# Performance work log

Hardware: AMD Instinct MI355X
Metric: run time of the kernel (lower is better)

## Reference

```python
import jax, jax.numpy as jnp
import numpy as np

DIM = 1024
HEADS = 16
DIM_HEAD = 64
INNER = HEADS * DIM_HEAD  # 1024
B, N = 4, 1024
SCALE = DIM_HEAD ** -0.5


def _layernorm(t, g, b, eps=1e-5):
    mu = jnp.mean(t, axis=-1, keepdims=True)
    var = jnp.var(t, axis=-1, keepdims=True)
    return (t - mu) * jax.lax.rsqrt(var + eps) * g + b


def setup_inputs() -> dict:
    key = jax.random.key(0)
    ks = jax.random.split(key, 8)
    return {
        "x": jax.random.normal(ks[0], (B, N, DIM), dtype=jnp.float32),
        "y": jax.random.normal(ks[1], (B, N, DIM), dtype=jnp.float32),
        "gx": jnp.ones((DIM,), jnp.float32),
        "bx": jnp.zeros((DIM,), jnp.float32),
        "gy": jnp.ones((DIM,), jnp.float32),
        "by": jnp.zeros((DIM,), jnp.float32),
        "Wqkv_x": jax.random.normal(ks[2], (DIM, 3 * INNER), jnp.float32) * 0.02,
        "Wqkv_y": jax.random.normal(ks[3], (DIM, 3 * INNER), jnp.float32) * 0.02,
        "Wout_x": jax.random.normal(ks[4], (INNER, DIM), jnp.float32) * 0.02,
        "bout_x": jnp.zeros((DIM,), jnp.float32),
        "Wout_y": jax.random.normal(ks[5], (INNER, DIM), jnp.float32) * 0.02,
        "bout_y": jnp.zeros((DIM,), jnp.float32),
    }


def _split_heads(t):
    b, n, _ = t.shape
    return t.reshape(b, n, HEADS, DIM_HEAD).transpose(0, 2, 1, 3)  # b h n d


def reference(x, y, gx, bx, gy, by, Wqkv_x, Wqkv_y, Wout_x, bout_x, Wout_y, bout_y):
    xn = _layernorm(x, gx, bx)
    yn = _layernorm(y, gy, by)
    qx, kx, vx = [_split_heads(t) for t in jnp.split(xn @ Wqkv_x, 3, axis=-1)]
    qy, ky, vy = [_split_heads(t) for t in jnp.split(yn @ Wqkv_y, 3, axis=-1)]
    # concat along HEADS dim -> 2h heads; each stream's heads attend within that stream
    q = jnp.concatenate([qx, qy], axis=1)
    k = jnp.concatenate([kx, ky], axis=1)
    v = jnp.concatenate([vx, vy], axis=1)
    dots = jnp.einsum('bhid,bhjd->bhij', q, k) * SCALE  # [B, 2h, N, N]
    attn = jax.nn.softmax(dots, axis=-1)
    out = jnp.einsum('bhij,bhjd->bhid', attn, v)  # [B, 2h, N, d]
    xo = out[:, :HEADS]  # original code uses the x-chunk for BOTH outputs (faithful)
    xo = xo.transpose(0, 2, 1, 3).reshape(xo.shape[0], xo.shape[2], INNER)  # b n (h d)
    out_x = xo @ Wout_x + bout_x
    out_y = xo @ Wout_y + bout_y
    return (out_x, out_y)
```

## Files before the change

### kernel.cpp

```cpp
#include <hip/hip_runtime.h>

typedef __attribute__((ext_vector_type(8))) short s16x8;
typedef __attribute__((ext_vector_type(4))) float f32x4;
typedef unsigned short u16;

#define DEV __device__ __forceinline__

DEV u16 f2bf(float f) {
    unsigned u = __builtin_bit_cast(unsigned, f);
    unsigned r = u + 0x7fffu + ((u >> 16) & 1u);
    return (u16)(r >> 16);
}

DEV float exp2a(float x) {
    float r;
    asm("v_exp_f32 %0, %1" : "=v"(r) : "v"(x));
    return r;
}

DEV unsigned cvtpk(float lo, float hi) {
    unsigned r;
    asm("v_cvt_pk_bf16_f32 %0, %1, %2" : "=v"(r) : "v"(lo), "v"(hi));
    return r;
}

DEV void gload_lds16(const void* g, void* l) {
    __builtin_amdgcn_global_load_lds(
        (const __attribute__((address_space(1))) unsigned int*)g,
        (__attribute__((address_space(3))) unsigned int*)l, 16, 0, 0);
}

DEV f32x4 mfma16(s16x8 a, s16x8 b, f32x4 c) {
    return __builtin_amdgcn_mfma_f32_16x16x32_bf16(a, b, c, 0, 0, 0);
}

template <int N>
DEV void vmwait() {
    asm volatile("s_waitcnt vmcnt(%0)" ::"n"(N) : "memory");
}

__global__ __launch_bounds__(256) void ln_kernel(const float* __restrict__ x,
                                                 const float* __restrict__ g,
                                                 const float* __restrict__ b,
                                                 u16* __restrict__ xn) {
    const int row = blockIdx.x, t = threadIdx.x;
    const float4 v = *(const float4*)(x + (size_t)row * 1024 + t * 4);
    float s1 = v.x + v.y + v.z + v.w;
    float s2 = v.x * v.x + v.y * v.y + v.z * v.z + v.w * v.w;
#pragma unroll
    for (int d = 1; d < 64; d <<= 1) {
        s1 += __shfl_xor(s1, d);
        s2 += __shfl_xor(s2, d);
    }
    __shared__ float red[8];
    if ((t & 63) == 0) { red[(t >> 6) * 2] = s1; red[(t >> 6) * 2 + 1] = s2; }
    __syncthreads();
    s1 = red[0] + red[2] + red[4] + red[6];
    s2 = red[1] + red[3] + red[5] + red[7];
    const float mu = s1 * (1.0f / 1024.0f);
    const float var = s2 * (1.0f / 1024.0f) - mu * mu;
    const float rs = rsqrtf(var + 1e-5f);
    const float4 gv = *(const float4*)(g + t * 4);
    const float4 bv = *(const float4*)(b + t * 4);
    ushort4 o;
    o.x = f2bf((v.x - mu) * rs * gv.x + bv.x);
    o.y = f2bf((v.y - mu) * rs * gv.y + bv.y);
    o.z = f2bf((v.z - mu) * rs * gv.z + bv.z);
    o.w = f2bf((v.w - mu) * rs * gv.w + bv.w);
    *(ushort4*)(xn + (size_t)row * 1024 + t * 4) = o;
}

__global__ __launch_bounds__(256) void transpose_w(const float* __restrict__ src0,
                                                   const float* __restrict__ src1,
                                                   u16* __restrict__ dst, int ld) {
    __shared__ float tile[64][68];
    const int t = threadIdx.x;
    const float* src = (blockIdx.z == 0) ? src0 : src1;
    u16* d0 = dst + (size_t)blockIdx.z * 1024 * 1024;
    const int n0 = blockIdx.x * 64, k0 = blockIdx.y * 64;
    const int kl = t >> 4, nl = (t & 15) * 4;
#pragma unroll
    for (int p = 0; p < 4; ++p) {
        float4 v = *(const float4*)(src + (size_t)(k0 + kl + p * 16) * ld + n0 + nl);
        tile[kl + p * 16][nl + 0] = v.x;
        tile[kl + p * 16][nl + 1] = v.y;
        tile[kl + p * 16][nl + 2] = v.z;
        tile[kl + p * 16][nl + 3] = v.w;
    }
    __syncthreads();
    const int nl2 = t >> 2, kc = (t & 3) * 16;
    __align__(16) u16 tmp[16];
#pragma unroll
    for (int j = 0; j < 16; ++j) tmp[j] = f2bf(tile[kc + j][nl2]);
    u16* d = d0 + (size_t)(n0 + nl2) * 1024 + k0 + kc;
    ((uint4*)d)[0] = ((const uint4*)tmp)[0];
    ((uint4*)d)[1] = ((const uint4*)tmp)[1];
}

__global__ __launch_bounds__(256) void transpose_v(const u16* __restrict__ V,
                                                   u16* __restrict__ Vt) {
    __shared__ u16 tile[64][72];
    const int t = threadIdx.x;
    const int j0 = blockIdx.x * 64;
    const int bh = blockIdx.y;
    const u16* src = V + (size_t)bh * 65536;
    const int jl = t >> 4, dl = (t & 15) * 4;
#pragma unroll
    for (int p = 0; p < 4; ++p) {
        ushort4 v = *(const ushort4*)(src + (size_t)(j0 + jl + p * 16) * 64 + dl);
        *(ushort4*)&tile[jl + p * 16][dl] = v;
    }
    __syncthreads();
    const int dl2 = t >> 2, jc = (t & 3) * 16;
    __align__(16) u16 tmp[16];
#pragma unroll
    for (int j = 0; j < 16; ++j) tmp[j] = tile[jc + j][dl2];
    u16* d = Vt + (size_t)bh * 65536 + (size_t)dl2 * 1024 + j0 + jc;
    ((uint4*)d)[0] = ((const uint4*)tmp)[0];
    ((uint4*)d)[1] = ((const uint4*)tmp)[1];
}

__global__ __launch_bounds__(512, 2) void gemm1k(const u16* __restrict__ A,
                                                 const u16* __restrict__ B,
                                                 u16* __restrict__ Qb, u16* __restrict__ Kb,
                                                 u16* __restrict__ Vb) {
    constexpr int MQ = 2, NQ = 3, HA = 32, HB = 48, TM = 64, TN = 96;
    constexpr int CHA = 1024, CHBF = 1536;
    constexpr int NI = 8;

    __shared__ __align__(16) u16 As[2 * 2 * CHA * 8];
    __shared__ __align__(16) u16 Bs[2 * CHBF * 8];

    const int tid = threadIdx.x, lane = tid & 63;
    const int wave = tid >> 6;
    const int wm = wave >> 1, wn = wave & 1;
    const int lr = lane & 15, cg = lane >> 4;

    const int bid = blockIdx.x;
    const int bid2 = (bid & 7) * 32 + (bid >> 3);
    const int bxi = bid2 & 15, byi = bid2 >> 4;
    const int m0 = byi * 256, n0 = bxi * 192;

    const u16* __restrict__ Ag = A + (size_t)m0 * 1024;
    const u16* __restrict__ Bg = B + (size_t)n0 * 1024;

    f32x4 acc[2 * MQ][2 * NQ] = {};

#define STG_A(b, h, t)                                                              \
    do {                                                                            \
        _Pragma("unroll") for (int u = 0; u < 2; ++u) {                             \
            const int idx = u * 512 + tid;                                          \
            const int loc = idx >> 3, pp = idx & 7;                                 \
            const int row = (loc & 127) | ((h)*128);                                \
            gload_lds16(Ag + (size_t)row * 1024 + (t)*64 + ((pp ^ (row & 7)) << 3), \
                        &As[(((b)*2 + (h)) * CHA + idx) * 8]);                      \
        }                                                                           \
    } while (0)
#define STG_B(b, t)                                                                 \
    do {                                                                            \
        _Pragma("unroll") for (int u = 0; u < 3; ++u) {                             \
            const int idx = u * 512 + tid;                                          \
            const int row = idx >> 3, pp = idx & 7;                                 \
            gload_lds16(Bg + (size_t)row * 1024 + (t)*64 + ((pp ^ (row & 7)) << 3), \
                        &Bs[((b)*CHBF + idx) * 8]);                                 \
        }                                                                           \
    } while (0)

#define LDA(bb, lm, dst)                                                            \
    _Pragma("unroll") for (int mf = 0; mf < MQ; ++mf)                               \
        _Pragma("unroll") for (int ks = 0; ks < 2; ++ks) {                          \
            const int grow = wm * 64 + (lm)*32 + mf * 16 + lr;                      \
            dst[mf][ks] = *(const s16x8*)&As[((((bb)*2 + (grow >> 7)) * CHA) +      \
                                              (grow & 127) * 8 +                    \
                                              ((cg + ks * 4) ^ (lr & 7))) * 8];     \
        }

#define LDB(bb, ln, dst)                                                            \
    _Pragma("unroll") for (int nf = 0; nf < NQ; ++nf)                               \
        _Pragma("unroll") for (int ks = 0; ks < 2; ++ks) {                          \
            const int rr = wn * TN + (ln)*HB + nf * 16 + lr;                        \
            dst[nf][ks] = *(const s16x8*)&Bs[((bb)*CHBF + rr * 8 +                  \
                                              ((cg + ks * 4) ^ (lr & 7))) * 8];     \
        }

#define MM(lm, ln, A_, B_)                                                          \
    __builtin_amdgcn_s_setprio(1);                                                  \
    _Pragma("unroll") for (int mf = 0; mf < MQ; ++mf)                               \
        _Pragma("unroll") for (int nf = 0; nf < NQ; ++nf)                           \
            _Pragma("unroll") for (int ks = 0; ks < 2; ++ks)                        \
                acc[(lm)*MQ + mf][(ln)*NQ + nf] = mfma16(                           \
                    A_[mf][ks], B_[nf][ks], acc[(lm)*MQ + mf][(ln)*NQ + nf]);       \
    __builtin_amdgcn_s_setprio(0);

#define BAR() asm volatile("s_barrier" ::: "memory")

    STG_A(0, 0, 0);
    STG_A(0, 1, 0);
    STG_B(0, 0);
    STG_A(1, 0, 1);
    STG_B(1, 1);
    vmwait<5>();
    BAR();

    s16x8 va[MQ][2];
    s16x8 vb0[NQ][2], vb1[NQ][2];

#pragma unroll 1
    for (int i = 0; i < NI - 1; ++i) {
        const int t1 = 2 * i + 1, t2 = 2 * i + 2, t3 = 2 * i + 3;
        LDA(0, 0, va); LDB(0, 0, vb0); STG_A(1, 1, t1); BAR(); MM(0, 0, va, vb0);
        LDB(0, 1, vb1);                                 BAR(); MM(0, 1, va, vb1);
        LDA(0, 1, va);                 STG_A(0, 0, t2); BAR(); MM(1, 0, va, vb0);
        STG_B(0, t2); vmwait<5>();                      BAR(); MM(1, 1, va, vb1);
        LDA(1, 0, va); LDB(1, 0, vb0); STG_A(0, 1, t2); BAR(); MM(0, 0, va, vb0);
        LDB(1, 1, vb1);                                 BAR(); MM(0, 1, va, vb1);
        LDA(1, 1, va);                 STG_A(1, 0, t3); BAR(); MM(1, 0, va, vb0);
        STG_B(1, t3); vmwait<5>();                      BAR(); MM(1, 1, va, vb1);
    }
    LDA(0, 0, va); LDB(0, 0, vb0); STG_A(1, 1, 15); BAR(); MM(0, 0, va, vb0);
    LDB(0, 1, vb1);                                 BAR(); MM(0, 1, va, vb1);
    LDA(0, 1, va);                                  BAR(); MM(1, 0, va, vb0);
    vmwait<0>();                                    BAR(); MM(1, 1, va, vb1);
    LDA(1, 0, va); LDB(1, 0, vb0); MM(0, 0, va, vb0);
    LDB(1, 1, vb1);                MM(0, 1, va, vb1);
    LDA(1, 1, va);                 MM(1, 0, va, vb0);
    MM(1, 1, va, vb1);

#undef STG_A
#undef STG_B
#undef LDA
#undef LDB
#undef MM
#undef BAR

#pragma unroll
    for (int am = 0; am < 2 * MQ; ++am) {
        const int lm = am / MQ, mf = am % MQ;
        const int rowb = m0 + wm * TM + lm * HA + mf * 16 + cg * 4;
#pragma unroll
        for (int an = 0; an < 2 * NQ; ++an) {
            const int ln = an / NQ, nf = an % NQ;
            const int col = n0 + wn * TN + ln * HB + nf * 16 + lr;
            const int which = col >> 10, hd = col & 1023;
            const int h = hd >> 6, dd = hd & 63;
            u16* dst = (which == 0) ? Qb : (which == 1) ? Kb : Vb;
            const float sc = (which == 0) ? 0.18033688011112042f : 1.0f;
#pragma unroll
            for (int r = 0; r < 4; ++r) {
                const int tk = rowb + r;
                const int bb2 = tk >> 10, ii = tk & 1023;
                dst[(size_t)(((bb2 << 4) + h) * 1024 + ii) * 64 + dd] =
                    f2bf(acc[am][an][r] * sc);
            }
        }
    }
}

template <int BN, int WM, int EPI>
__global__ __launch_bounds__(512, 2) void gemm8(const u16* __restrict__ A,
                                                const u16* __restrict__ B,
                                                u16* __restrict__ Qb, u16* __restrict__ Kb,
                                                u16* __restrict__ Vb,
                                                const float* __restrict__ bx,
                                                const float* __restrict__ by,
                                                float* __restrict__ out, int NBX) {
    constexpr int BM = 256, WN = 8 / WM;
    constexpr int TM = BM / WM, TN = BN / WN;
    constexpr int MQ = TM / 32, NQ = TN / 32;
    constexpr int HA = TM / 2, HB = TN / 2;
    constexpr int CHA = 1024;
    constexpr int CHB = BN * 4;
    constexpr int GA = 2, GB = CHB / 512;
    constexpr int NI = 8;

    __shared__ __align__(16) u16 As[2 * 2 * CHA * 8];
    __shared__ __align__(16) u16 Bs[2 * 2 * CHB * 8];

    const int tid = threadIdx.x, lane = tid & 63;
    const int wave = tid >> 6;
    const int wm = wave / WN, wn = wave % WN;
    const int lr = lane & 15, cg = lane >> 4;

    const int nwg = NBX * 16;
    const int bid = blockIdx.x;
    const int bid2 = (bid & 7) * (nwg >> 3) + (bid >> 3);
    const int bxi = bid2 % NBX, byi = bid2 / NBX;
    const int m0 = byi * 256, n0 = bxi * BN;

    const u16* __restrict__ Ag = A + (size_t)m0 * 1024;
    const u16* __restrict__ Bg = B + (size_t)n0 * 1024;

    f32x4 acc[2 * MQ][2 * NQ] = {};

#define STG_A(b, h, t)                                                              \
    do {                                                                            \
        _Pragma("unroll") for (int u = 0; u < GA; ++u) {                            \
            const int idx = u * 512 + tid;                                          \
            const int loc = idx >> 3, pp = idx & 7;                                 \
            const int row = (loc & (HA - 1)) | ((h)*HA) | ((loc / HA) * 2 * HA);    \
            gload_lds16(Ag + (size_t)row * 1024 + (t)*64 + ((pp ^ (row & 7)) << 3), \
                        &As[(((b)*2 + (h)) * CHA + idx) * 8]);                      \
        }                                                                           \
    } while (0)
#define STG_B(b, h, t)                                                              \
    do {                                                                            \
        _Pragma("unroll") for (int u = 0; u < GB; ++u) {                            \
            const int idx = u * 512 + tid;                                          \
            const int loc = idx >> 3, pp = idx & 7;                                 \
            const int row = (loc & (HB - 1)) | ((h)*HB) | ((loc / HB) * 2 * HB);    \
            gload_lds16(Bg + (size_t)row * 1024 + (t)*64 + ((pp ^ (row & 7)) << 3), \
                        &Bs[(((b)*2 + (h)) * CHB + idx) * 8]);                      \
        }                                                                           \
    } while (0)

#define LDA(bb, lm, dst)                                                            \
    _Pragma("unroll") for (int mf = 0; mf < MQ; ++mf)                               \
        _Pragma("unroll") for (int ks = 0; ks < 2; ++ks)                            \
            dst[mf][ks] = *(const s16x8*)&As[((((bb)*2 + (lm)) * CHA) +             \
                                              (mf * 16 + lr + wm * HA) * 8 +        \
                                              ((cg + ks * 4) ^ (lr & 7))) * 8];

#define LDB(bb, ln, dst)                                                            \
    _Pragma("unroll") for (int nf = 0; nf < NQ; ++nf)                               \
        _Pragma("unroll") for (int ks = 0; ks < 2; ++ks)                            \
            dst[nf][ks] = *(const s16x8*)&Bs[((((bb)*2 + (ln)) * CHB) +             \
                                              (nf * 16 + lr + wn * HB) * 8 +        \
                                              ((cg + ks * 4) ^ (lr & 7))) * 8];

#define MM(lm, ln, A_, B_)                                                          \
    __builtin_amdgcn_s_setprio(1);                                                  \
    _Pragma("unroll") for (int mf = 0; mf < MQ; ++mf)                               \
        _Pragma("unroll") for (int nf = 0; nf < NQ; ++nf)                           \
            _Pragma("unroll") for (int ks = 0; ks < 2; ++ks)                        \
                acc[(lm)*MQ + mf][(ln)*NQ + nf] = mfma16(                           \
                    A_[mf][ks], B_[nf][ks], acc[(lm)*MQ + mf][(ln)*NQ + nf]);       \
    __builtin_amdgcn_s_setprio(0);

#define BAR() asm volatile("s_barrier" ::: "memory")

    STG_A(0, 0, 0);
    STG_A(0, 1, 0);
    STG_B(0, 0, 0);
    STG_B(0, 1, 0);
    STG_A(1, 0, 1);
    STG_B(1, 0, 1);
    vmwait<GA + GB>();
    BAR();

    s16x8 va[MQ][2];
    s16x8 vb0[NQ][2], vb1[NQ][2];

#pragma unroll 1
    for (int i = 0; i < NI - 1; ++i) {
        const int t1 = 2 * i + 1, t2 = 2 * i + 2, t3 = 2 * i + 3;
        LDA(0, 0, va); LDB(0, 0, vb0); STG_A(1, 1, t1); BAR(); MM(0, 0, va, vb0);
        LDB(0, 1, vb1);                STG_B(1, 1, t1); BAR(); MM(0, 1, va, vb1);
        LDA(0, 1, va);                 STG_A(0, 0, t2); BAR(); MM(1, 0, va, vb0);
        STG_B(0, 0, t2); vmwait<GA + GB>();             BAR(); MM(1, 1, va, vb1);
        LDA(1, 0, va); LDB(1, 0, vb0); STG_A(0, 1, t2); BAR(); MM(0, 0, va, vb0);
        LDB(1, 1, vb1);                STG_B(0, 1, t2); BAR(); MM(0, 1, va, vb1);
        LDA(1, 1, va);                 STG_A(1, 0, t3); BAR(); MM(1, 0, va, vb0);
        STG_B(1, 0, t3); vmwait<GA + GB>();             BAR(); MM(1, 1, va, vb1);
    }
    LDA(0, 0, va); LDB(0, 0, vb0); STG_A(1, 1, 15); BAR(); MM(0, 0, va, vb0);
    LDB(0, 1, vb1);                STG_B(1, 1, 15); BAR(); MM(0, 1, va, vb1);
    LDA(0, 1, va);                                  BAR(); MM(1, 0, va, vb0);
    vmwait<0>();                                    BAR(); MM(1, 1, va, vb1);
    LDA(1, 0, va); LDB(1, 0, vb0); MM(0, 0, va, vb0);
    LDB(1, 1, vb1);                MM(0, 1, va, vb1);
    LDA(1, 1, va);                 MM(1, 0, va, vb0);
    MM(1, 1, va, vb1);

#undef STG_A
#undef STG_B
#undef LDA
#undef LDB
#undef MM
#undef BAR

#pragma unroll
    for (int am = 0; am < 2 * MQ; ++am) {
        const int lm = am / MQ, mf = am % MQ;
        const int rowb = m0 + wm * TM + lm * HA + mf * 16 + cg * 4;
#pragma unroll
        for (int an = 0; an < 2 * NQ; ++an) {
            const int ln = an / NQ, nf = an % NQ;
            const int col = n0 + wn * TN + ln * HB + nf * 16 + lr;
            if (EPI == 0) {
                const int which = col >> 10, hd = col & 1023;
                const int h = hd >> 6, dd = hd & 63;
                u16* dst = (which == 0) ? Qb : (which == 1) ? Kb : Vb;
                const float sc = (which == 0) ? 0.18033688011112042f : 1.0f;
#pragma unroll
                for (int r = 0; r < 4; ++r) {
                    const int tk = rowb + r;
                    const int bb2 = tk >> 10, ii = tk & 1023;
                    dst[(size_t)(((bb2 << 4) + h) * 1024 + ii) * 64 + dd] =
                        f2bf(acc[am][an][r] * sc);
                }
            } else {
                float bias;
                float* ob;
                if (col < 1024) { bias = bx[col]; ob = out + col; }
                else { bias = by[col - 1024]; ob = out + 4194304 + (col - 1024); }
#pragma unroll
                for (int r = 0; r < 4; ++r)
                    ob[(size_t)(rowb + r) * 1024] = acc[am][an][r] + bias;
            }
        }
    }
}

__global__ __launch_bounds__(256) void attn_kernel(const u16* __restrict__ Q,
                                                   const u16* __restrict__ Kg,
                                                   const u16* __restrict__ Vt,
                                                   u16* __restrict__ xo) {
    __shared__ __align__(16) u16 Ks[3][64 * 64];
    __shared__ __align__(16) u16 Vs[3][64 * 64];
    __shared__ __align__(16) u16 Ps[4][32 * 64];
    const int tid = threadIdx.x, lane = tid & 63, w = tid >> 6;
    const int bid = blockIdx.x;
    const int bh = (bid & 7) * 8 + ((bid >> 3) & 7);
    const int qblk = bid >> 6;
    const u16* Qh = Q + (size_t)bh * 65536;
    const u16* Kh = Kg + (size_t)bh * 65536;
    const u16* Vh = Vt + (size_t)bh * 65536;
    const int lr = lane & 15, cg = lane >> 4;
    const int q0 = qblk * 128 + w * 32;
    u16* Pw = &Ps[w][0];

    s16x8 qf[2][2];
#pragma unroll
    for (int qg = 0; qg < 2; ++qg)
#pragma unroll
        for (int ks = 0; ks < 2; ++ks)
            qf[qg][ks] =
                *(const s16x8*)(Qh + (size_t)(q0 + qg * 16 + lr) * 64 + ks * 32 + cg * 8);

    f32x4 o[2][4] = {};
    float l_s[2] = {0.f, 0.f};
    float m_s[2] = {-3e38f, -3e38f};
    int ba[4];
#pragma unroll
    for (int r = 0; r < 4; ++r) ba[r] = (cg * 4 + r) * 4;

#define STAGEKV(bufi, kv0)                                                               \
    do {                                                                                 \
        _Pragma("unroll") for (int i = 0; i < 2; ++i) {                                  \
            int idx = i * 256 + tid;                                                     \
            int row = idx >> 3, p = idx & 7;                                             \
            gload_lds16(Kh + (size_t)((kv0) + row) * 64 + ((p ^ (row & 7)) << 3),        \
                        &Ks[bufi][idx * 8]);                                             \
            gload_lds16(Vh + (size_t)row * 1024 + (kv0) + ((p ^ (row & 7)) << 3),        \
                        &Vs[bufi][idx * 8]);                                             \
        }                                                                                \
    } while (0)

    STAGEKV(0, 0);
    STAGEKV(1, 64);

    int buf = 0, sbuf = 2;
    for (int t = 0; t < 16; ++t) {
        if (t == 15) { vmwait<0>(); } else { vmwait<4>(); }
        asm volatile("s_barrier" ::: "memory");
        if (t < 14) STAGEKV(sbuf, (t + 2) * 64);

        f32x4 s[2][4] = {};
#pragma unroll
        for (int fn = 0; fn < 4; ++fn) {
            const int r = fn * 16 + lr;
#pragma unroll
            for (int ks = 0; ks < 2; ++ks) {
                const int c = cg + ks * 4;
                s16x8 kf = *(const s16x8*)&Ks[buf][r * 64 + ((c ^ (r & 7)) << 3)];
                s[0][fn] = mfma16(kf, qf[0][ks], s[0][fn]);
                s[1][fn] = mfma16(kf, qf[1][ks], s[1][fn]);
            }
        }

#pragma unroll
        for (int qg = 0; qg < 2; ++qg) {
            float tm = -3e38f;
#pragma unroll
            for (int fn = 0; fn < 4; ++fn)
#pragma unroll
                for (int r = 0; r < 4; ++r) tm = fmaxf(tm, s[qg][fn][r]);
            tm = fmaxf(tm, __shfl_xor(tm, 16));
            tm = fmaxf(tm, __shfl_xor(tm, 32));
            if (!__all(tm <= m_s[qg] + 8.0f)) {
                const float mn = fmaxf(m_s[qg], tm);
                const float corr = exp2a(m_s[qg] - mn);
                m_s[qg] = mn;
                l_s[qg] *= corr;
                f32x4 corr_o;
#pragma unroll
                for (int r = 0; r < 4; ++r)
                    corr_o[r] = __builtin_bit_cast(
                        float,
                        __builtin_amdgcn_ds_bpermute(ba[r], __builtin_bit_cast(int, corr)));
#pragma unroll
                for (int fd = 0; fd < 4; ++fd) o[qg][fd] *= corr_o;
            }
            const float mn = m_s[qg];
            float rs = 0.f;
            const int prow = (qg * 16 + lr) * 64;
#pragma unroll
            for (int fn = 0; fn < 4; ++fn) {
                const float p0 = exp2a(s[qg][fn][0] - mn);
                const float p1 = exp2a(s[qg][fn][1] - mn);
                const float p2 = exp2a(s[qg][fn][2] - mn);
                const float p3 = exp2a(s[qg][fn][3] - mn);
                rs += (p0 + p1) + (p2 + p3);
                uint2 dd;
                dd.x = cvtpk(p0, p1);
                dd.y = cvtpk(p2, p3);
                *(uint2*)(Pw + prow + (((2 * fn + (cg >> 1)) ^ (lr & 7)) << 3) +
                          ((cg & 1) << 2)) = dd;
            }
            rs += __shfl_xor(rs, 16);
            rs += __shfl_xor(rs, 32);
            l_s[qg] += rs;
        }

        s16x8 pf[2][2];
#pragma unroll
        for (int qg = 0; qg < 2; ++qg)
#pragma unroll
            for (int ks = 0; ks < 2; ++ks)
                pf[qg][ks] = *(const s16x8*)(Pw + (qg * 16 + lr) * 64 +
                                             (((4 * ks + cg) ^ (lr & 7)) << 3));
#pragma unroll
        for (int fd = 0; fd < 4; ++fd) {
            const int rr = fd * 16 + lr;
#pragma unroll
            for (int ks = 0; ks < 2; ++ks) {
                const int c = cg + ks * 4;
                s16x8 vf = *(const s16x8*)&Vs[buf][rr * 64 + ((c ^ (rr & 7)) << 3)];
                o[0][fd] = mfma16(pf[0][ks], vf, o[0][fd]);
                o[1][fd] = mfma16(pf[1][ks], vf, o[1][fd]);
            }
        }
        buf = (buf == 2) ? 0 : buf + 1;
        sbuf = (sbuf == 2) ? 0 : sbuf + 1;
    }
#undef STAGEKV

    const int b = bh >> 4, h = bh & 15;
#pragma unroll
    for (int qg = 0; qg < 2; ++qg) {
        f32x4 inv;
#pragma unroll
        for (int r = 0; r < 4; ++r) {
            const float lq = __builtin_bit_cast(
                float, __builtin_amdgcn_ds_bpermute(ba[r], __builtin_bit_cast(int, l_s[qg])));
            inv[r] = 1.0f / lq;
        }
#pragma unroll
        for (int r = 0; r < 4; ++r) {
            const int qrow = q0 + qg * 16 + cg * 4 + r;
#pragma unroll
            for (int fd = 0; fd < 4; ++fd)
                xo[(size_t)(b * 1024 + qrow) * 1024 + h * 64 + fd * 16 + lr] =
                    f2bf(o[qg][fd][r] * inv[r]);
        }
    }
}

extern "C" void kernel_launch(void* const* d_in, const int* in_sizes, int n_in,
                              void* d_out, int out_size, void* d_ws, size_t ws_size,
                              hipStream_t stream) {
    const float* x = (const float*)d_in[0];
    const float* gx = (const float*)d_in[2];
    const float* bxv = (const float*)d_in[3];
    const float* Wqkv = (const float*)d_in[6];
    const float* Woutx = (const float*)d_in[8];
    const float* boutx = (const float*)d_in[9];
    const float* Wouty = (const float*)d_in[10];
    const float* bouty = (const float*)d_in[11];
    float* out = (float*)d_out;

    u16* ws = (u16*)d_ws;
    u16* xn = ws;
    u16* wqkv_t = xn + 4096 * 1024;
    u16* wout_t = wqkv_t + 3072 * 1024;
    u16* Qb = wout_t + 2048 * 1024;
    u16* Kb = Qb + 64 * 1024 * 64;
    u16* Vb = Kb + 64 * 1024 * 64;
    u16* Vtb = Vb + 64 * 1024 * 64;
    u16* xob = Vtb + 64 * 1024 * 64;

    ln_kernel<<<4096, 256, 0, stream>>>(x, gx, bxv, xn);
    transpose_w<<<dim3(48, 16, 1), 256, 0, stream>>>(Wqkv, nullptr, wqkv_t, 3072);
    transpose_w<<<dim3(16, 16, 2), 256, 0, stream>>>(Woutx, Wouty, wout_t, 1024);
    gemm1k<<<256, 512, 0, stream>>>(xn, wqkv_t, Qb, Kb, Vb);
    transpose_v<<<dim3(16, 64), 256, 0, stream>>>(Vb, Vtb);
    attn_kernel<<<512, 256, 0, stream>>>(Qb, Kb, Vtb, xob);
    gemm8<128, 4, 1><<<256, 512, 0, stream>>>(xob, wout_t, nullptr, nullptr, nullptr,
                                              boutx, bouty, out, 16);
}
```

Measured before the change: 106.1 us.

## Merge layernorm and weight transposes into one kernel; write V transposed from QKV GEMM

Folds the layernorm kernel and both weight-transpose launches into a single prep kernel that dispatches on block index. It also removes the separate V transpose kernel: the QKV GEMM epilogue now writes V directly in transposed [bh][d][n] layout using 4-element packed stores. This cuts three kernel launches and a full read/write pass over V. The trade-off is that the Q/K scatter stays unchanged and the V stores are strided across d rows.

```diff
diff --git a/kernel.cpp b/kernel.cpp
--- a/kernel.cpp
+++ b/kernel.cpp
@@ -39,45 +39,59 @@
     asm volatile("s_waitcnt vmcnt(%0)" ::"n"(N) : "memory");
 }
 
-__global__ __launch_bounds__(256) void ln_kernel(const float* __restrict__ x,
-                                                 const float* __restrict__ g,
-                                                 const float* __restrict__ b,
-                                                 u16* __restrict__ xn) {
-    const int row = blockIdx.x, t = threadIdx.x;
-    const float4 v = *(const float4*)(x + (size_t)row * 1024 + t * 4);
-    float s1 = v.x + v.y + v.z + v.w;
-    float s2 = v.x * v.x + v.y * v.y + v.z * v.z + v.w * v.w;
-#pragma unroll
-    for (int d = 1; d < 64; d <<= 1) {
-        s1 += __shfl_xor(s1, d);
-        s2 += __shfl_xor(s2, d);
-    }
-    __shared__ float red[8];
-    if ((t & 63) == 0) { red[(t >> 6) * 2] = s1; red[(t >> 6) * 2 + 1] = s2; }
-    __syncthreads();
-    s1 = red[0] + red[2] + red[4] + red[6];
-    s2 = red[1] + red[3] + red[5] + red[7];
-    const float mu = s1 * (1.0f / 1024.0f);
-    const float var = s2 * (1.0f / 1024.0f) - mu * mu;
-    const float rs = rsqrtf(var + 1e-5f);
-    const float4 gv = *(const float4*)(g + t * 4);
-    const float4 bv = *(const float4*)(b + t * 4);
-    ushort4 o;
-    o.x = f2bf((v.x - mu) * rs * gv.x + bv.x);
-    o.y = f2bf((v.y - mu) * rs * gv.y + bv.y);
-    o.z = f2bf((v.z - mu) * rs * gv.z + bv.z);
-    o.w = f2bf((v.w - mu) * rs * gv.w + bv.w);
-    *(ushort4*)(xn + (size_t)row * 1024 + t * 4) = o;
-}
-
-__global__ __launch_bounds__(256) void transpose_w(const float* __restrict__ src0,
-                                                   const float* __restrict__ src1,
-                                                   u16* __restrict__ dst, int ld) {
+__global__ __launch_bounds__(256) void prep_kernel(
+    const float* __restrict__ x, const float* __restrict__ g,
+    const float* __restrict__ b, u16* __restrict__ xn,
+    const float* __restrict__ Wqkv, const float* __restrict__ Woutx,
+    const float* __restrict__ Wouty, u16* __restrict__ wqkv_t,
+    u16* __restrict__ wout_t) {
     __shared__ float tile[64][68];
     const int t = threadIdx.x;
-    const float* src = (blockIdx.z == 0) ? src0 : src1;
-    u16* d0 = dst + (size_t)blockIdx.z * 1024 * 1024;
-    const int n0 = blockIdx.x * 64, k0 = blockIdx.y * 64;
+    const int bid = blockIdx.x;
+
+    if (bid < 4096) {
+        const int row = bid;
+        const float4 v = *(const float4*)(x + (size_t)row * 1024 + t * 4);
+        float s1 = v.x + v.y + v.z + v.w;
+        float s2 = v.x * v.x + v.y * v.y + v.z * v.z + v.w * v.w;
+#pragma unroll
+        for (int d = 1; d < 64; d <<= 1) {
+            s1 += __shfl_xor(s1, d);
+            s2 += __shfl_xor(s2, d);
+        }
+        float* red = &tile[0][0];
+        if ((t & 63) == 0) { red[(t >> 6) * 2] = s1; red[(t >> 6) * 2 + 1] = s2; }
+        __syncthreads();
+        s1 = red[0] + red[2] + red[4] + red[6];
+        s2 = red[1] + red[3] + red[5] + red[7];
+        const float mu = s1 * (1.0f / 1024.0f);
+        const float var = s2 * (1.0f / 1024.0f) - mu * mu;
+        const float rs = rsqrtf(var + 1e-5f);
+        const float4 gv = *(const float4*)(g + t * 4);
+        const float4 bv = *(const float4*)(b + t * 4);
+        ushort4 o;
+        o.x = f2bf((v.x - mu) * rs * gv.x + bv.x);
+        o.y = f2bf((v.y - mu) * rs * gv.y + bv.y);
+        o.z = f2bf((v.z - mu) * rs * gv.z + bv.z);
+        o.w = f2bf((v.w - mu) * rs * gv.w + bv.w);
+        *(ushort4*)(xn + (size_t)row * 1024 + t * 4) = o;
+        return;
+    }
+
+    const float* src;
+    u16* d0;
+    int ld, n0, k0;
+    if (bid < 4096 + 768) {
+        const int idx = bid - 4096;
+        src = Wqkv; d0 = wqkv_t; ld = 3072;
+        n0 = (idx % 48) * 64; k0 = (idx / 48) * 64;
+    } else {
+        const int idx = bid - 4096 - 768;
+        const int z = idx >> 8, rem = idx & 255;
+        src = (z == 0) ? Woutx : Wouty;
+        d0 = wout_t + (size_t)z * 1024 * 1024; ld = 1024;
+        n0 = (rem & 15) * 64; k0 = (rem >> 4) * 64;
+    }
     const int kl = t >> 4, nl = (t & 15) * 4;
 #pragma unroll
     for (int p = 0; p < 4; ++p) {
@@ -97,33 +111,10 @@
     ((uint4*)d)[1] = ((const uint4*)tmp)[1];
 }
 
-__global__ __launch_bounds__(256) void transpose_v(const u16* __restrict__ V,
-                                                   u16* __restrict__ Vt) {
-    __shared__ u16 tile[64][72];
-    const int t = threadIdx.x;
-    const int j0 = blockIdx.x * 64;
-    const int bh = blockIdx.y;
-    const u16* src = V + (size_t)bh * 65536;
-    const int jl = t >> 4, dl = (t & 15) * 4;
-#pragma unroll
-    for (int p = 0; p < 4; ++p) {
-        ushort4 v = *(const ushort4*)(src + (size_t)(j0 + jl + p * 16) * 64 + dl);
-        *(ushort4*)&tile[jl + p * 16][dl] = v;
-    }
-    __syncthreads();
-    const int dl2 = t >> 2, jc = (t & 3) * 16;
-    __align__(16) u16 tmp[16];
-#pragma unroll
-    for (int j = 0; j < 16; ++j) tmp[j] = tile[jc + j][dl2];
-    u16* d = Vt + (size_t)bh * 65536 + (size_t)dl2 * 1024 + j0 + jc;
-    ((uint4*)d)[0] = ((const uint4*)tmp)[0];
-    ((uint4*)d)[1] = ((const uint4*)tmp)[1];
-}
-
 __global__ __launch_bounds__(512, 2) void gemm1k(const u16* __restrict__ A,
                                                  const u16* __restrict__ B,
                                                  u16* __restrict__ Qb, u16* __restrict__ Kb,
-                                                 u16* __restrict__ Vb) {
+                                                 u16* __restrict__ Vt) {
     constexpr int MQ = 2, NQ = 3, HA = 32, HB = 48, TM = 64, TN = 96;
     constexpr int CHA = 1024, CHBF = 1536;
     constexpr int NI = 8;
@@ -237,20 +228,27 @@
     for (int am = 0; am < 2 * MQ; ++am) {
         const int lm = am / MQ, mf = am % MQ;
         const int rowb = m0 + wm * TM + lm * HA + mf * 16 + cg * 4;
+        const int bb2 = rowb >> 10, ii = rowb & 1023;
 #pragma unroll
         for (int an = 0; an < 2 * NQ; ++an) {
             const int ln = an / NQ, nf = an % NQ;
             const int col = n0 + wn * TN + ln * HB + nf * 16 + lr;
             const int which = col >> 10, hd = col & 1023;
             const int h = hd >> 6, dd = hd & 63;
-            u16* dst = (which == 0) ? Qb : (which == 1) ? Kb : Vb;
-            const float sc = (which == 0) ? 0.18033688011112042f : 1.0f;
-#pragma unroll
-            for (int r = 0; r < 4; ++r) {
-                const int tk = rowb + r;
-                const int bb2 = tk >> 10, ii = tk & 1023;
-                dst[(size_t)(((bb2 << 4) + h) * 1024 + ii) * 64 + dd] =
-                    f2bf(acc[am][an][r] * sc);
+            if (which == 2) {
+                ushort4 pk;
+                pk.x = f2bf(acc[am][an][0]);
+                pk.y = f2bf(acc[am][an][1]);
+                pk.z = f2bf(acc[am][an][2]);
+                pk.w = f2bf(acc[am][an][3]);
+                *(ushort4*)(Vt + (size_t)((bb2 << 4) + h) * 65536 + dd * 1024 + ii) = pk;
+            } else {
+                u16* dst = (which == 0) ? Qb : Kb;
+                const float sc = (which == 0) ? 0.18033688011112042f : 1.0f;
+#pragma unroll
+                for (int r = 0; r < 4; ++r)
+                    dst[(size_t)(((bb2 << 4) + h) * 1024 + ii + r) * 64 + dd] =
+                        f2bf(acc[am][an][r] * sc);
             }
         }
     }
@@ -585,15 +583,12 @@
     u16* wout_t = wqkv_t + 3072 * 1024;
     u16* Qb = wout_t + 2048 * 1024;
     u16* Kb = Qb + 64 * 1024 * 64;
-    u16* Vb = Kb + 64 * 1024 * 64;
-    u16* Vtb = Vb + 64 * 1024 * 64;
+    u16* Vtb = Kb + 64 * 1024 * 64;
     u16* xob = Vtb + 64 * 1024 * 64;
 
-    ln_kernel<<<4096, 256, 0, stream>>>(x, gx, bxv, xn);
-    transpose_w<<<dim3(48, 16, 1), 256, 0, stream>>>(Wqkv, nullptr, wqkv_t, 3072);
-    transpose_w<<<dim3(16, 16, 2), 256, 0, stream>>>(Woutx, Wouty, wout_t, 1024);
-    gemm1k<<<256, 512, 0, stream>>>(xn, wqkv_t, Qb, Kb, Vb);
-    transpose_v<<<dim3(16, 64), 256, 0, stream>>>(Vb, Vtb);
+    prep_kernel<<<4096 + 768 + 512, 256, 0, stream>>>(x, gx, bxv, xn, Wqkv, Woutx,
+                                                      Wouty, wqkv_t, wout_t);
+    gemm1k<<<256, 512, 0, stream>>>(xn, wqkv_t, Qb, Kb, Vtb);
     attn_kernel<<<512, 256, 0, stream>>>(Qb, Kb, Vtb, xob);
     gemm8<128, 4, 1><<<256, 512, 0, stream>>>(xob, wout_t, nullptr, nullptr, nullptr,
                                               boutx, bouty, out, 16);
```

Result: faster. 99.16 us (-6.6%).
